# Performance work log

Measured on AMD Instinct MI355X. Metric: run time of the kernel, lower is better.

## Reference

```python
import jax, jax.numpy as jnp
import numpy as np


def setup_inputs() -> dict:
    key = jax.random.key(0)
    ks = jax.random.split(key, 5)
    B, T, D, U = 32, 2048, 512, 512
    scale = 1.0 / np.sqrt(D)
    return {
        "full": jax.random.normal(ks[0], (B, T, D), jnp.float32),
        "last": jax.random.normal(ks[1], (B, D), jnp.float32),
        "W1": jax.random.normal(ks[2], (D, U), jnp.float32) * scale,
        "b1": jnp.zeros((U,), jnp.float32),
        "W2": jax.random.normal(ks[3], (D, U), jnp.float32) * scale,
        "b2": jnp.zeros((U,), jnp.float32),
        "V": jax.random.normal(ks[4], (U, 1), jnp.float32) * (1.0 / np.sqrt(U)),
        "bV": jnp.zeros((1,), jnp.float32),
    }


def reference(full, last, W1, b1, W2, b2, V, bV):
    # full: [B,T,D], last: [B,D]
    h1 = jnp.einsum("btd,du->btu", full, W1) + b1          # [B,T,U]
    h2 = last @ W2 + b2                                      # [B,U]
    score = jnp.tanh(h1 + h2[:, None, :]) @ V + bV           # [B,T,1]
    attn = jax.nn.softmax(score, axis=1)                     # [B,T,1]
    context = jnp.sum(attn * full, axis=1)                   # [B,D]
    return context
```

## Files before the change

### kernel.cpp

```cpp
#include <hip/hip_runtime.h>
#include <math.h>


#define BB 32
#define TT 2048
#define DD 512
#define UU 512

typedef short bf16x8 __attribute__((ext_vector_type(8)));
typedef float f32x4  __attribute__((ext_vector_type(4)));

static __device__ __forceinline__ short f2bf(float f) {
    unsigned x = __float_as_uint(f);
    return (short)((x + 0x7fffu + ((x >> 16) & 1u)) >> 16);
}

static __device__ __forceinline__ float fast_tanh(float x) {
    float e = __expf(2.f * x);
    return 1.f - 2.f * __builtin_amdgcn_rcpf(e + 1.f);
}

__global__ __launch_bounds__(256) void prep_kernel(const float* __restrict__ W1,
                                                   short* __restrict__ W1T,
                                                   const float* __restrict__ last,
                                                   const float* __restrict__ W2,
                                                   const float* __restrict__ b1,
                                                   const float* __restrict__ b2,
                                                   float* __restrict__ h2) {
    __shared__ float tile[32][33];
    __shared__ float ls[DD];
    const int bid = blockIdx.x;
    const int tid = threadIdx.x;
    if (bid < 256) {
        const int tr = (bid >> 4) << 5;
        const int tc = (bid & 15) << 5;
#pragma unroll
        for (int p = 0; p < 4; ++p) {
            const int r = p * 8 + (tid >> 5), c = tid & 31;
            tile[r][c] = W1[(size_t)(tr + r) * UU + tc + c];
        }
        __syncthreads();
#pragma unroll
        for (int p = 0; p < 4; ++p) {
            const int r = p * 8 + (tid >> 5), c = tid & 31;
            W1T[(size_t)(tc + r) * DD + tr + c] = f2bf(tile[c][r]);
        }
    } else {
        const int b = bid - 256;
        for (int i = tid; i < DD; i += 256) ls[i] = last[b * DD + i];
        __syncthreads();
        float a0 = 0.f, a1 = 0.f;
#pragma unroll 8
        for (int d = 0; d < DD; ++d) {
            const float l = ls[d];
            a0 += l * W2[d * UU + tid];
            a1 += l * W2[d * UU + tid + 256];
        }
        h2[b * UU + tid]       = a0 + b1[tid] + b2[tid];
        h2[b * UU + tid + 256] = a1 + b1[tid + 256] + b2[tid + 256];
    }
}

__global__ __launch_bounds__(256, 2) void score_kernel(const float* __restrict__ full,
                                                       const short* __restrict__ W1T,
                                                       const float* __restrict__ h2,
                                                       const float* __restrict__ V,
                                                       float* __restrict__ scores) {
    __shared__ __align__(16) float a32[64 * 32];
    __shared__ __align__(16) short blds[512 * 32];
    __shared__ float score_red[4][64];

    const int bid = blockIdx.x;
    const int b  = bid >> 5;
    const int t0 = (bid & 31) << 6;
    const int tid = threadIdx.x;
    const int w    = tid >> 6;
    const int lane = tid & 63;
    const int quad = lane >> 4;
    const int col  = lane & 15;

    f32x4 acc[4][8];
#pragma unroll
    for (int i = 0; i < 4; ++i)
#pragma unroll
        for (int j = 0; j < 8; ++j) acc[i][j] = (f32x4){0.f, 0.f, 0.f, 0.f};

    const size_t fullbase = (size_t)(b * TT + t0) * DD;

    for (int ko = 0; ko < 16; ++ko) {
        if (ko) __syncthreads();
#pragma unroll
        for (int i = 0; i < 2; ++i) {
            const int id = w * 128 + i * 64 + lane;
            const int r  = id >> 3;
            const int cc = (id & 7) ^ (r & 7);
            const float* g = &full[fullbase + (size_t)r * DD + ko * 32 + cc * 4];
            __builtin_amdgcn_global_load_lds(
                (const __attribute__((address_space(1))) void*)g,
                (__attribute__((address_space(3))) void*)&a32[(w * 128 + i * 64) * 4],
                16, 0, 0);
        }
#pragma unroll
        for (int i = 0; i < 8; ++i) {
            const int id = w * 512 + i * 64 + lane;
            const int u  = id >> 2;
            const int kc = (id & 3) ^ (u & 3) ^ ((u >> 2) & 3);
            const short* g = &W1T[(size_t)u * DD + ko * 32 + kc * 8];
            __builtin_amdgcn_global_load_lds(
                (const __attribute__((address_space(1))) void*)g,
                (__attribute__((address_space(3))) void*)&blds[(w * 512 + i * 64) * 8],
                16, 0, 0);
        }
        __syncthreads();

        bf16x8 af[4];
#pragma unroll
        for (int mt = 0; mt < 4; ++mt) {
            const int r = mt * 16 + col;
            const f32x4 lo = *(const f32x4*)&a32[(r * 8 + ((quad * 2 + 0) ^ (r & 7))) * 4];
            const f32x4 hi = *(const f32x4*)&a32[(r * 8 + ((quad * 2 + 1) ^ (r & 7))) * 4];
            af[mt] = (bf16x8){f2bf(lo.x), f2bf(lo.y), f2bf(lo.z), f2bf(lo.w),
                              f2bf(hi.x), f2bf(hi.y), f2bf(hi.z), f2bf(hi.w)};
        }
#pragma unroll
        for (int nt = 0; nt < 8; ++nt) {
            const int u  = w * 128 + nt * 16 + col;
            const int sl = u * 4 + (quad ^ (u & 3) ^ ((u >> 2) & 3));
            const bf16x8 bf = *(const bf16x8*)&blds[sl * 8];
#pragma unroll
            for (int mt = 0; mt < 4; ++mt)
                acc[mt][nt] = __builtin_amdgcn_mfma_f32_16x16x32_bf16(af[mt], bf, acc[mt][nt], 0, 0, 0);
        }
    }

    float srow[16];
#pragma unroll
    for (int i = 0; i < 16; ++i) srow[i] = 0.f;
#pragma unroll
    for (int nt = 0; nt < 8; ++nt) {
        const int u = w * 128 + nt * 16 + col;
        const float hv = h2[b * UU + u];
        const float vv = V[u];
#pragma unroll
        for (int mt = 0; mt < 4; ++mt)
#pragma unroll
            for (int r = 0; r < 4; ++r)
                srow[mt * 4 + r] += fast_tanh(acc[mt][nt][r] + hv) * vv;
    }
#pragma unroll
    for (int off = 1; off < 16; off <<= 1) {
#pragma unroll
        for (int i = 0; i < 16; ++i) srow[i] += __shfl_xor(srow[i], off, 64);
    }
    if (col == 0) {
#pragma unroll
        for (int mt = 0; mt < 4; ++mt)
#pragma unroll
            for (int r = 0; r < 4; ++r)
                score_red[w][mt * 16 + quad * 4 + r] = srow[mt * 4 + r];
    }
    __syncthreads();
    if (tid < 64)
        scores[b * TT + t0 + tid] = score_red[0][tid] + score_red[1][tid] +
                                    score_red[2][tid] + score_red[3][tid];
}

__global__ __launch_bounds__(256) void context_kernel(const float* __restrict__ full,
                                                      const float* __restrict__ scores,
                                                      float* __restrict__ out) {
    const int bid = blockIdx.x;
    const int b  = bid >> 3;
    const int d0 = ((bid >> 1) & 3) * 128;
    const int t0 = (bid & 1) * 1024;
    const int tid = threadIdx.x;
    const int c  = tid & 31;
    const int tr = tid >> 5;

    __shared__ float red[256];
    __shared__ float ps[1024];
    __shared__ float4 red4[256];

    float local[8];
    float m = -1e30f;
#pragma unroll
    for (int j = 0; j < 8; ++j) {
        local[j] = scores[b * TT + j * 256 + tid];
        m = fmaxf(m, local[j]);
    }
    red[tid] = m;
    __syncthreads();
    for (int s = 128; s > 0; s >>= 1) {
        if (tid < s) red[tid] = fmaxf(red[tid], red[tid + s]);
        __syncthreads();
    }
    const float mx = red[0];
    __syncthreads();

    float sum = 0.f;
    float e[8];
#pragma unroll
    for (int j = 0; j < 8; ++j) {
        e[j] = __expf(local[j] - mx);
        sum += e[j];
    }
    const int jbase = t0 >> 8;
#pragma unroll
    for (int i = 0; i < 4; ++i) ps[i * 256 + tid] = e[jbase + i];
    red[tid] = sum;
    __syncthreads();
    for (int s = 128; s > 0; s >>= 1) {
        if (tid < s) red[tid] += red[tid + s];
        __syncthreads();
    }
    const float inv = 1.f / red[0];

    float ax = 0.f, ay = 0.f, az = 0.f, aw = 0.f;
    const float* base = full + ((size_t)(b * TT + t0)) * DD + d0;
#pragma unroll 4
    for (int it = 0; it < 128; ++it) {
        const int t = it * 8 + tr;
        const float4 v = *(const float4*)&base[(size_t)t * DD + c * 4];
        const float wg = ps[t];
        ax += wg * v.x; ay += wg * v.y; az += wg * v.z; aw += wg * v.w;
    }
    red4[tid] = make_float4(ax, ay, az, aw);
    __syncthreads();
    if (tid < 32) {
        float4 s = red4[tid];
#pragma unroll
        for (int g = 1; g < 8; ++g) {
            const float4 o = red4[g * 32 + tid];
            s.x += o.x; s.y += o.y; s.z += o.z; s.w += o.w;
        }
        atomicAdd(&out[b * DD + d0 + tid * 4 + 0], s.x * inv);
        atomicAdd(&out[b * DD + d0 + tid * 4 + 1], s.y * inv);
        atomicAdd(&out[b * DD + d0 + tid * 4 + 2], s.z * inv);
        atomicAdd(&out[b * DD + d0 + tid * 4 + 3], s.w * inv);
    }
}

extern "C" void kernel_launch(void* const* d_in, const int* in_sizes, int n_in,
                              void* d_out, int out_size, void* d_ws, size_t ws_size,
                              hipStream_t stream) {
    const float* full = (const float*)d_in[0];
    const float* last = (const float*)d_in[1];
    const float* W1   = (const float*)d_in[2];
    const float* b1   = (const float*)d_in[3];
    const float* W2   = (const float*)d_in[4];
    const float* b2   = (const float*)d_in[5];
    const float* V    = (const float*)d_in[6];

    float* out    = (float*)d_out;
    float* scores = (float*)d_ws;
    float* h2     = (float*)d_ws + (size_t)BB * TT;
    short* W1T    = (short*)(h2 + (size_t)BB * UU);

    hipMemsetAsync(d_out, 0, (size_t)out_size * sizeof(float), stream);
    prep_kernel<<<256 + BB, 256, 0, stream>>>(W1, W1T, last, W2, b1, b2, h2);
    score_kernel<<<BB * (TT / 64), 256, 0, stream>>>(full, W1T, h2, V, scores);
    context_kernel<<<256, 256, 0, stream>>>(full, scores, out);
}
```

Before: 300.1 us.

## Split score kernel over U halves, widen context/h2 grids, fold memsets into prep

The score kernel now splits the U dimension into two halves per block, which doubles the grid and halves the accumulator registers and B-tile LDS. Partial scores are combined with atomicAdd into a scores buffer that the prep kernel zeroes. The h2 projection is spread over 128 blocks instead of 32, the context kernel uses 512 blocks with shorter T slices, and the output memset moves into prep. The cost is that each score block re-reads its 64x512 tile of the full input twice, plus the extra atomics.

```diff
diff --git a/kernel.cpp b/kernel.cpp
--- a/kernel.cpp
+++ b/kernel.cpp
@@ -26,9 +26,12 @@
                                                    const float* __restrict__ W2,
                                                    const float* __restrict__ b1,
                                                    const float* __restrict__ b2,
-                                                   float* __restrict__ h2) {
+                                                   float* __restrict__ h2,
+                                                   float* __restrict__ scores,
+                                                   float* __restrict__ out) {
     __shared__ float tile[32][33];
     __shared__ float ls[DD];
+    __shared__ float part[256];
     const int bid = blockIdx.x;
     const int tid = threadIdx.x;
     if (bid < 256) {
@@ -45,19 +48,30 @@
             const int r = p * 8 + (tid >> 5), c = tid & 31;
             W1T[(size_t)(tc + r) * DD + tr + c] = f2bf(tile[c][r]);
         }
+    } else if (bid < 384) {
+        const int b2i = bid - 256;
+        const int b  = b2i >> 2;
+        const int u0 = (b2i & 3) << 7;
+        for (int i = tid; i < DD; i += 256) ls[i] = last[b * DD + i];
+        __syncthreads();
+        const int uu = tid & 127;
+        const int dh = tid >> 7;
+        float acc = 0.f;
+#pragma unroll 8
+        for (int d = dh * 256; d < dh * 256 + 256; ++d)
+            acc += ls[d] * W2[d * UU + u0 + uu];
+        part[tid] = acc;
+        __syncthreads();
+        if (tid < 128) {
+            const int u = u0 + tid;
+            h2[b * UU + u] = part[tid] + part[tid + 128] + b1[u] + b2[u];
+        }
+    } else if (bid == 384) {
+        float4 z = make_float4(0.f, 0.f, 0.f, 0.f);
+        for (int i = tid; i < (BB * TT) / 4; i += 256) ((float4*)scores)[i] = z;
     } else {
-        const int b = bid - 256;
-        for (int i = tid; i < DD; i += 256) ls[i] = last[b * DD + i];
-        __syncthreads();
-        float a0 = 0.f, a1 = 0.f;
-#pragma unroll 8
-        for (int d = 0; d < DD; ++d) {
-            const float l = ls[d];
-            a0 += l * W2[d * UU + tid];
-            a1 += l * W2[d * UU + tid + 256];
-        }
-        h2[b * UU + tid]       = a0 + b1[tid] + b2[tid];
-        h2[b * UU + tid + 256] = a1 + b1[tid + 256] + b2[tid + 256];
+        float4 z = make_float4(0.f, 0.f, 0.f, 0.f);
+        for (int i = tid; i < (BB * DD) / 4; i += 256) ((float4*)out)[i] = z;
     }
 }
 
@@ -67,23 +81,24 @@
                                                        const float* __restrict__ V,
                                                        float* __restrict__ scores) {
     __shared__ __align__(16) float a32[64 * 32];
-    __shared__ __align__(16) short blds[512 * 32];
+    __shared__ __align__(16) short blds[256 * 32];
     __shared__ float score_red[4][64];
 
     const int bid = blockIdx.x;
-    const int b  = bid >> 5;
-    const int t0 = (bid & 31) << 6;
+    const int b  = bid >> 6;
+    const int t0 = ((bid >> 1) & 31) << 6;
+    const int u0 = (bid & 1) << 8;
     const int tid = threadIdx.x;
     const int w    = tid >> 6;
     const int lane = tid & 63;
     const int quad = lane >> 4;
     const int col  = lane & 15;
 
-    f32x4 acc[4][8];
+    f32x4 acc[4][4];
 #pragma unroll
     for (int i = 0; i < 4; ++i)
 #pragma unroll
-        for (int j = 0; j < 8; ++j) acc[i][j] = (f32x4){0.f, 0.f, 0.f, 0.f};
+        for (int j = 0; j < 4; ++j) acc[i][j] = (f32x4){0.f, 0.f, 0.f, 0.f};
 
     const size_t fullbase = (size_t)(b * TT + t0) * DD;
 
@@ -101,14 +116,14 @@
                 16, 0, 0);
         }
 #pragma unroll
-        for (int i = 0; i < 8; ++i) {
-            const int id = w * 512 + i * 64 + lane;
-            const int u  = id >> 2;
-            const int kc = (id & 3) ^ (u & 3) ^ ((u >> 2) & 3);
-            const short* g = &W1T[(size_t)u * DD + ko * 32 + kc * 8];
+        for (int i = 0; i < 4; ++i) {
+            const int id = w * 256 + i * 64 + lane;
+            const int ul = id >> 2;
+            const int kc = (id & 3) ^ (ul & 3) ^ ((ul >> 2) & 3);
+            const short* g = &W1T[(size_t)(u0 + ul) * DD + ko * 32 + kc * 8];
             __builtin_amdgcn_global_load_lds(
                 (const __attribute__((address_space(1))) void*)g,
-                (__attribute__((address_space(3))) void*)&blds[(w * 512 + i * 64) * 8],
+                (__attribute__((address_space(3))) void*)&blds[(w * 256 + i * 64) * 8],
                 16, 0, 0);
         }
         __syncthreads();
@@ -123,9 +138,9 @@
                               f2bf(hi.x), f2bf(hi.y), f2bf(hi.z), f2bf(hi.w)};
         }
 #pragma unroll
-        for (int nt = 0; nt < 8; ++nt) {
-            const int u  = w * 128 + nt * 16 + col;
-            const int sl = u * 4 + (quad ^ (u & 3) ^ ((u >> 2) & 3));
+        for (int nt = 0; nt < 4; ++nt) {
+            const int ul = w * 64 + nt * 16 + col;
+            const int sl = ul * 4 + (quad ^ (ul & 3) ^ ((ul >> 2) & 3));
             const bf16x8 bf = *(const bf16x8*)&blds[sl * 8];
 #pragma unroll
             for (int mt = 0; mt < 4; ++mt)
@@ -137,8 +152,8 @@
 #pragma unroll
     for (int i = 0; i < 16; ++i) srow[i] = 0.f;
 #pragma unroll
-    for (int nt = 0; nt < 8; ++nt) {
-        const int u = w * 128 + nt * 16 + col;
+    for (int nt = 0; nt < 4; ++nt) {
+        const int u = u0 + w * 64 + nt * 16 + col;
         const float hv = h2[b * UU + u];
         const float vv = V[u];
 #pragma unroll
@@ -161,23 +176,23 @@
     }
     __syncthreads();
     if (tid < 64)
-        scores[b * TT + t0 + tid] = score_red[0][tid] + score_red[1][tid] +
-                                    score_red[2][tid] + score_red[3][tid];
+        atomicAdd(&scores[b * TT + t0 + tid],
+                  score_red[0][tid] + score_red[1][tid] + score_red[2][tid] + score_red[3][tid]);
 }
 
 __global__ __launch_bounds__(256) void context_kernel(const float* __restrict__ full,
                                                       const float* __restrict__ scores,
                                                       float* __restrict__ out) {
     const int bid = blockIdx.x;
-    const int b  = bid >> 3;
-    const int d0 = ((bid >> 1) & 3) * 128;
-    const int t0 = (bid & 1) * 1024;
+    const int b  = bid >> 4;
+    const int d0 = ((bid >> 2) & 3) << 7;
+    const int t0 = (bid & 3) << 9;
     const int tid = threadIdx.x;
     const int c  = tid & 31;
     const int tr = tid >> 5;
 
     __shared__ float red[256];
-    __shared__ float ps[1024];
+    __shared__ float ps[512];
     __shared__ float4 red4[256];
 
     float local[8];
@@ -203,9 +218,9 @@
         e[j] = __expf(local[j] - mx);
         sum += e[j];
     }
-    const int jbase = t0 >> 8;
-#pragma unroll
-    for (int i = 0; i < 4; ++i) ps[i * 256 + tid] = e[jbase + i];
+    const int jb = (bid & 3) * 2;
+#pragma unroll
+    for (int i = 0; i < 2; ++i) ps[i * 256 + tid] = e[jb + i];
     red[tid] = sum;
     __syncthreads();
     for (int s = 128; s > 0; s >>= 1) {
@@ -217,7 +232,7 @@
     float ax = 0.f, ay = 0.f, az = 0.f, aw = 0.f;
     const float* base = full + ((size_t)(b * TT + t0)) * DD + d0;
 #pragma unroll 4
-    for (int it = 0; it < 128; ++it) {
+    for (int it = 0; it < 64; ++it) {
         const int t = it * 8 + tr;
         const float4 v = *(const float4*)&base[(size_t)t * DD + c * 4];
         const float wg = ps[t];
@@ -255,8 +270,7 @@
     float* h2     = (float*)d_ws + (size_t)BB * TT;
     short* W1T    = (short*)(h2 + (size_t)BB * UU);
 
-    hipMemsetAsync(d_out, 0, (size_t)out_size * sizeof(float), stream);
-    prep_kernel<<<256 + BB, 256, 0, stream>>>(W1, W1T, last, W2, b1, b2, h2);
-    score_kernel<<<BB * (TT / 64), 256, 0, stream>>>(full, W1T, h2, V, scores);
-    context_kernel<<<256, 256, 0, stream>>>(full, scores, out);
-}
+    prep_kernel<<<386, 256, 0, stream>>>(W1, W1T, last, W2, b1, b2, h2, scores, out);
+    score_kernel<<<BB * (TT / 64) * 2, 256, 0, stream>>>(full, W1T, h2, V, scores);
+    context_kernel<<<512, 256, 0, stream>>>(full, scores, out);
+}
```

Measured after the change: 293.2 us. -2.3%, faster.
